# Optimization experiments

Hardware: AMD Instinct MI355X
Metric: run time of the kernel (lower is better)

Reference implementation:

```python
import jax, jax.numpy as jnp
import numpy as np

TEMP = 0.01  # temperature_att_sc


def grid_sample_bilinear(img, grid):
    """torch.nn.functional.grid_sample, mode='bilinear', padding_mode='zeros',
    align_corners=False. img: (B,C,H,W); grid: (B,Hg,Wg,2) with (x,y) coords."""
    B, C, H, W = img.shape
    gx, gy = grid[..., 0], grid[..., 1]            # (B,Hg,Wg)
    ix = ((gx + 1.0) * W - 1.0) * 0.5              # unnormalize (align_corners=False)
    iy = ((gy + 1.0) * H - 1.0) * 0.5
    ix0 = jnp.floor(ix); iy0 = jnp.floor(iy)
    ix1 = ix0 + 1.0;     iy1 = iy0 + 1.0
    wx1 = ix - ix0; wx0 = 1.0 - wx1
    wy1 = iy - iy0; wy0 = 1.0 - wy1
    flat = img.reshape(B, C, H * W)
    Hg, Wg = gx.shape[1], gx.shape[2]

    def gather(iy_, ix_):
        valid = (ix_ >= 0) & (ix_ <= W - 1) & (iy_ >= 0) & (iy_ <= H - 1)
        ixc = jnp.clip(ix_, 0, W - 1).astype(jnp.int32)
        iyc = jnp.clip(iy_, 0, H - 1).astype(jnp.int32)
        idx = (iyc * W + ixc).reshape(B, 1, Hg * Wg)
        vals = jnp.take_along_axis(flat, jnp.broadcast_to(idx, (B, C, Hg * Wg)), axis=2)
        vals = vals.reshape(B, C, Hg, Wg)
        return vals * valid[:, None, :, :].astype(img.dtype)

    out = (gather(iy0, ix0) * (wy0 * wx0)[:, None]
         + gather(iy0, ix1) * (wy0 * wx1)[:, None]
         + gather(iy1, ix0) * (wy1 * wx0)[:, None]
         + gather(iy1, ix1) * (wy1 * wx1)[:, None])
    return out


def setup_inputs() -> dict:
    key = jax.random.key(0)
    ks = jax.random.split(key, 16)
    B, S, D = 256, 197, 768
    H60 = 60
    std = 0.02
    inp = {
        "x": jax.random.normal(ks[0], (B, S, D), dtype=jnp.float32),
        "mask": jnp.zeros((B, S), dtype=jnp.float32),
        "Wq": jax.random.normal(ks[1], (D, D), dtype=jnp.float32) * std,
        "bq": jnp.zeros((D,), dtype=jnp.float32),
        "Wk": jax.random.normal(ks[2], (D, D), dtype=jnp.float32) * std,
        "bk": jnp.zeros((D,), dtype=jnp.float32),
        "Wv": jax.random.normal(ks[3], (D, D), dtype=jnp.float32) * std,
        "bv": jnp.zeros((D,), dtype=jnp.float32),
        "W1": jax.random.normal(ks[4], (H60, 2 * D), dtype=jnp.float32) * std,
        "b1": jnp.zeros((H60,), dtype=jnp.float32),
        "W2": jax.random.normal(ks[5], (H60, H60), dtype=jnp.float32) * std,
        "b2": jnp.zeros((H60,), dtype=jnp.float32),
        "W3": jax.random.normal(ks[6], (2, H60), dtype=jnp.float32) * std,
        "b3": jnp.zeros((2,), dtype=jnp.float32),
    }
    return inp


def reference(x, mask, Wq, bq, Wk, bk, Wv, bv, W1, b1, W2, b2, W3, b3):
    B, S, D = x.shape
    G = int(np.sqrt(S))  # grid_dim; S = G*G + 1 (class token)
    q = jnp.einsum('bsd,ed->bse', x, Wq) + bq
    k = jnp.einsum('bsd,ed->bse', x, Wk) + bk
    v = jnp.einsum('bsd,ed->bse', x, Wv) + bv
    k_nc = k[:, 1:, :]          # (B, G*G, D)
    v_nc = v[:, 1:, :]
    q_nc = q[:, 1:, :]
    k_img = jnp.transpose(k_nc, (0, 2, 1)).reshape(B, D, G, G)
    v_img = jnp.transpose(v_nc, (0, 2, 1)).reshape(B, D, G, G)
    # key_net_2D MLP -> per-patch sampling offsets in [0,1]
    h = jnp.concatenate((q_nc, k_nc), axis=2)       # (B, G*G, 2D)
    h = jax.nn.relu(jnp.einsum('bse,fe->bsf', h, W1) + b1)
    h = jax.nn.relu(jnp.einsum('bse,fe->bsf', h, W2) + b2)
    sample = jax.nn.sigmoid(jnp.einsum('bse,fe->bsf', h, W3) + b3)  # (B, G*G, 2)
    sample_x = sample[:, :, 0:1]
    sample_y = sample[:, :, 1:2]
    grid = jnp.concatenate((sample_x, sample_y), axis=1).reshape(B, G, G, 2)
    sk = grid_sample_bilinear(k_img, grid)          # (B, D, G, G)
    sv = grid_sample_bilinear(v_img, grid)
    sk = jnp.transpose(sk.reshape(B, D, G * G), (0, 2, 1))  # (B, G*G, D)
    sv = jnp.transpose(sv.reshape(B, D, G * G), (0, 2, 1))
    cls = jnp.ones((B, 1, D), dtype=x.dtype)
    sk = jnp.concatenate((cls, sk), axis=1)         # (B, S, D)
    sv = jnp.concatenate((cls, sv), axis=1)
    scores = jnp.sum(sk * q, axis=-1)               # (B, S)
    attention = jax.nn.sigmoid(TEMP * scores)[:, :, None] * sv
    return attention
```

## Files before the change

kernel.cpp:

```cpp
#include <hip/hip_runtime.h>
#include <hip/hip_bf16.h>
#include <stdint.h>

#define TEMP 0.01f

typedef __attribute__((ext_vector_type(8))) short short8;
typedef __attribute__((ext_vector_type(4))) float f32x4;
typedef __attribute__((ext_vector_type(2))) float f32x2;

__device__ __forceinline__ ushort f2bf(float f) {
  union { float f; uint32_t u; } c; c.f = f;
  uint32_t u = c.u;
  uint32_t r = (u + 0x7FFFu + ((u >> 16) & 1u)) >> 16;
  return (ushort)r;
}
__device__ __forceinline__ float bf2f(ushort h) {
  union { uint32_t u; float f; } c; c.u = ((uint32_t)h) << 16;
  return c.f;
}

__device__ __forceinline__ void async16(void* lds, const void* g) {
  __builtin_amdgcn_global_load_lds(
      (const __attribute__((address_space(1))) uint32_t*)g,
      (__attribute__((address_space(3))) uint32_t*)lds,
      16, 0, 0);
}

__global__ __launch_bounds__(256) void convert_all(
    const float* __restrict__ X, ushort* __restrict__ Xb,
    const float* __restrict__ Wq, const float* __restrict__ Wk, const float* __restrict__ Wv,
    const float* __restrict__ bq, const float* __restrict__ bk, const float* __restrict__ bv,
    const float* __restrict__ W1, const float* __restrict__ b1,
    ushort* __restrict__ wqkv, ushort* __restrict__ w1p,
    float* __restrict__ biasq, float* __restrict__ b1p) {
  int idx = blockIdx.x * 256 + threadIdx.x;
  int stride = gridDim.x * 256;
  for (int i = idx; i < 9682944; i += stride) {
    float4 f = ((const float4*)X)[i];
    ushort4 u;
    u.x = f2bf(f.x); u.y = f2bf(f.y); u.z = f2bf(f.z); u.w = f2bf(f.w);
    ((ushort4*)Xb)[i] = u;
  }
  for (int i = idx; i < 2304 * 768; i += stride) {
    int row = i / 768;
    float v = (row < 768) ? Wq[i] : (row < 1536) ? Wk[i - 768 * 768] : Wv[i - 1536 * 768];
    wqkv[i] = f2bf(v);
  }
  for (int i = idx; i < 64 * 1536; i += stride) {
    int row = i / 1536;
    w1p[i] = f2bf(row < 60 ? W1[i] : 0.f);
  }
  for (int i = idx; i < 2304; i += stride)
    biasq[i] = (i < 768) ? bq[i] : (i < 1536) ? bk[i - 768] : bv[i - 1536];
  for (int i = idx; i < 64; i += stride)
    b1p[i] = (i < 60) ? b1[i] : 0.f;
}

#define STAGE(LDSBASE, SRC, OFF)                                          \
  async16(smem + (LDSBASE) + ldsW, (SRC) + (OFF));                        \
  async16(smem + (LDSBASE) + 8192 + ldsW, (SRC) + 64 * 1536 + (OFF))

#define RDA4(BASE, F0)                                                                   \
  _Pragma("unroll") for (int f = 0; f < 4; ++f) {                                        \
    a[f][0] = *(const short8*)(smem + (BASE) + aRow + ((F0) + f) * 2048 + c0);           \
    a[f][1] = *(const short8*)(smem + (BASE) + aRow + ((F0) + f) * 2048 + c1);           \
  }
#define RDB2(BASE, G0)                                                                   \
  _Pragma("unroll") for (int g = 0; g < 2; ++g) {                                        \
    b[(G0) + g][0] = *(const short8*)(smem + (BASE) + bRow + ((G0) + g) * 2048 + c0);    \
    b[(G0) + g][1] = *(const short8*)(smem + (BASE) + bRow + ((G0) + g) * 2048 + c1);    \
  }
#define MF16(F0, G0)                                                                     \
  _Pragma("unroll") for (int f = 0; f < 4; ++f)                                          \
  _Pragma("unroll") for (int g = 0; g < 2; ++g) {                                        \
    acc[(F0) + f][(G0) + g] = __builtin_amdgcn_mfma_f32_16x16x32_bf16(                   \
        a[f][0], b[(G0) + g][0], acc[(F0) + f][(G0) + g], 0, 0, 0);                      \
    acc[(F0) + f][(G0) + g] = __builtin_amdgcn_mfma_f32_16x16x32_bf16(                   \
        a[f][1], b[(G0) + g][1], acc[(F0) + f][(G0) + g], 0, 0, 0);                      \
  }
#define PH_OPEN                                          \
  __builtin_amdgcn_s_barrier();                          \
  asm volatile("s_waitcnt lgkmcnt(0)" ::: "memory");     \
  __builtin_amdgcn_s_setprio(1);
#define PH_CLOSE                                         \
  __builtin_amdgcn_s_setprio(0);                         \
  __builtin_amdgcn_s_barrier();

__global__ __launch_bounds__(512, 1) void gemm_qkv(const ushort* __restrict__ Xb,
                                                   const ushort* __restrict__ Wb,
                                                   const float* __restrict__ bias,
                                                   ushort* __restrict__ QKV) {
  __shared__ char smem[131072];
  const int tid = threadIdx.x;
  const int lane = tid & 63;
  const int wv = tid >> 6;
  const int wr = wv >> 2;
  const int wc = wv & 3;
  const int lmod = lane & 15, ldiv = lane >> 4;

  int orig = blockIdx.x;
  int xcd = orig & 7, bidx = orig >> 3;
  int nw = (xcd < 5 ? xcd * 222 : 1110 + (xcd - 5) * 221) + bidx;
  const int m0 = (nw / 9) * 256;
  const int n0 = (nw % 9) * 256;

  const int srow = tid >> 3;
  const int scol = (((tid & 7) ^ (srow & 7)) << 4);
  const char* aS = (const char*)Xb + (size_t)(m0 + srow) * 1536 + scol;
  const char* bS = (const char*)Wb + (size_t)(n0 + srow) * 1536 + scol;
  const int ldsW = wv << 10;

  const int aRow = (wr * 128 + lmod) * 128;
  const int bRow = (wc * 64 + lmod) * 128;
  const int c0 = (ldiv * 16) ^ ((lmod & 7) << 4);
  const int c1 = (64 + ldiv * 16) ^ ((lmod & 7) << 4);

  const int AE = 0, AO = 32768, BE = 65536, BO = 98304;

  f32x4 acc[8][4] = {};

  STAGE(AE, aS, 0);
  STAGE(AE + 16384, aS + 128 * 1536, 0);
  STAGE(BE, bS, 0);
  STAGE(BE + 16384, bS + 128 * 1536, 0);
  STAGE(AO, aS, 128);
  asm volatile("s_waitcnt vmcnt(2)" ::: "memory");
  __builtin_amdgcn_s_barrier();

  for (int i = 0; i < 6; ++i) {
    const int kb1 = i * 256 + 128;
    const int kb2 = i * 256 + 256;
    const int kb3 = i * 256 + 384;
    const bool more = (i < 5);

    short8 a[4][2], b[4][2];
    RDA4(AE, 0); RDB2(BE, 0);
    STAGE(AO + 16384, aS + 128 * 1536, kb1);
    PH_OPEN; MF16(0, 0); PH_CLOSE;
    RDB2(BE, 2);
    STAGE(BO, bS, kb1);
    PH_OPEN; MF16(0, 2); PH_CLOSE;
    RDA4(AE, 4);
    STAGE(BO + 16384, bS + 128 * 1536, kb1);
    PH_OPEN; MF16(4, 0); PH_CLOSE;
    if (more) { STAGE(AE, aS, kb2); }
    PH_OPEN; MF16(4, 2);
    __builtin_amdgcn_s_setprio(0);
    if (more) { asm volatile("s_waitcnt vmcnt(2)" ::: "memory"); }
    else      { asm volatile("s_waitcnt vmcnt(0)" ::: "memory"); }
    __builtin_amdgcn_s_barrier();
    RDA4(AO, 0); RDB2(BO, 0);
    if (more) { STAGE(AE + 16384, aS + 128 * 1536, kb2); }
    PH_OPEN; MF16(0, 0); PH_CLOSE;
    RDB2(BO, 2);
    if (more) { STAGE(BE, bS, kb2); }
    PH_OPEN; MF16(0, 2); PH_CLOSE;
    RDA4(AO, 4);
    if (more) { STAGE(BE + 16384, bS + 128 * 1536, kb2); }
    PH_OPEN; MF16(4, 0); PH_CLOSE;
    if (more) { STAGE(AO, aS, kb3); }
    PH_OPEN; MF16(4, 2);
    __builtin_amdgcn_s_setprio(0);
    if (more) { asm volatile("s_waitcnt vmcnt(2)" ::: "memory"); }
    __builtin_amdgcn_s_barrier();
  }

#pragma unroll
  for (int f = 0; f < 8; ++f) {
    int row = m0 + wr * 128 + f * 16 + ldiv * 4;
#pragma unroll
    for (int g = 0; g < 4; ++g) {
      int col = n0 + wc * 64 + g * 16 + lmod;
      float bs = bias[col];
#pragma unroll
      for (int rr = 0; rr < 4; ++rr)
        QKV[(size_t)(row + rr) * 2304 + col] = f2bf(acc[f][g][rr] + bs);
    }
  }
}

__global__ __launch_bounds__(256) void gemm_mlp(const ushort* __restrict__ QKV,
                                                const ushort* __restrict__ W1p,
                                                const float* __restrict__ b1p,
                                                const float* __restrict__ W2,
                                                const float* __restrict__ b2,
                                                const float* __restrict__ W3,
                                                const float* __restrict__ b3,
                                                float* __restrict__ SAMPLE) {
  __shared__ char smem[32032];
  float* sW2 = (float*)(smem + 16896);
  float* sW3 = (float*)(smem + 31296);
  float* sb2 = (float*)(smem + 31776);
  float* sb3 = (float*)(smem + 32016);
  const int tid = threadIdx.x;
  const int lane = tid & 63;
  const int wv = tid >> 6;
  const int p0 = blockIdx.x * 128;
  const int lmod = lane & 15, ldiv = lane >> 4;

  for (int i = tid; i < 3600; i += 256) sW2[i] = W2[i];
  for (int i = tid; i < 120; i += 256) sW3[i] = W3[i];
  if (tid < 60) sb2[tid] = b2[tid];
  if (tid < 2) sb3[tid] = b3[tid];

  f32x4 acc[2][4] = {};
  const ushort* As = (const ushort*)smem;
  const ushort* Bs = (const ushort*)(smem + 8192);

  const int r = tid >> 2, cb = (tid & 3) * 16;
  int p_a = p0 + r;
  int p_b = p0 + 64 + r;
  int grow_a = (p_a / 196) * 197 + 1 + (p_a % 196);
  int grow_b = (p_b / 196) * 197 + 1 + (p_b % 196);
  const char* gA0 = (const char*)QKV + (size_t)grow_a * 4608 + cb;
  const char* gA1 = (const char*)QKV + (size_t)grow_b * 4608 + cb;
  const char* gB = (const char*)W1p + (size_t)r * 3072 + cb;

  for (int k0 = 0; k0 < 1536; k0 += 32) {
    int kb = k0 * 2;
    async16(smem + wv * 1024,        gA0 + kb);
    async16(smem + 4096 + wv * 1024, gA1 + kb);
    async16(smem + 8192 + wv * 1024, gB + kb);
    __syncthreads();

    short8 a[2], b[4];
    a[0] = *(const short8*)(As + (wv * 32 + lmod) * 32 + ldiv * 8);
    a[1] = *(const short8*)(As + (wv * 32 + 16 + lmod) * 32 + ldiv * 8);
#pragma unroll
    for (int j = 0; j < 4; ++j)
      b[j] = *(const short8*)(Bs + (j * 16 + lmod) * 32 + ldiv * 8);
#pragma unroll
    for (int i = 0; i < 2; ++i)
#pragma unroll
      for (int j = 0; j < 4; ++j)
        acc[i][j] = __builtin_amdgcn_mfma_f32_16x16x32_bf16(a[i], b[j], acc[i][j], 0, 0, 0);
    __syncthreads();
  }

  ushort* Hs = (ushort*)smem;
#pragma unroll
  for (int i = 0; i < 2; ++i) {
    int lrow = wv * 32 + i * 16 + ldiv * 4;
#pragma unroll
    for (int j = 0; j < 4; ++j) {
      int col = j * 16 + lmod;
      float bs = b1p[col];
#pragma unroll
      for (int rr = 0; rr < 4; ++rr) {
        float v = fmaxf(acc[i][j][rr] + bs, 0.f);
        Hs[(lrow + rr) * 66 + col] = f2bf(v);
      }
    }
  }
  __syncthreads();

  const int plocal = tid >> 1;
  const int half = tid & 1;
  const uint32_t* hrow = (const uint32_t*)(Hs + plocal * 66);
  float h[60];
#pragma unroll
  for (int i = 0; i < 30; ++i) {
    uint32_t u = hrow[i];
    h[2 * i] = bf2f((ushort)(u & 0xffffu));
    h[2 * i + 1] = bf2f((ushort)(u >> 16));
  }
  float s0 = 0.f, s1 = 0.f;
  const int obase = half * 30;
  for (int oo = 0; oo < 30; ++oo) {
    int o = obase + oo;
    float a = sb2[o];
    const float4* wrow = (const float4*)(sW2 + o * 60);
#pragma unroll
    for (int k = 0; k < 15; ++k) {
      float4 w4 = wrow[k];
      a += h[4 * k] * w4.x + h[4 * k + 1] * w4.y + h[4 * k + 2] * w4.z + h[4 * k + 3] * w4.w;
    }
    a = fmaxf(a, 0.f);
    s0 += a * sW3[o];
    s1 += a * sW3[60 + o];
  }
  s0 += __shfl_xor(s0, 1, 64);
  s1 += __shfl_xor(s1, 1, 64);
  if (half == 0) {
    int p = p0 + plocal;
    SAMPLE[2 * p]     = 1.f / (1.f + __expf(-(s0 + sb3[0])));
    SAMPLE[2 * p + 1] = 1.f / (1.f + __expf(-(s1 + sb3[1])));
  }
}

__global__ __launch_bounds__(256) void sample_attn(const ushort* __restrict__ QKV,
                                                   const float* __restrict__ SAMPLE,
                                                   float* __restrict__ OUT) {
  int tid = threadIdx.x, lane = tid & 63, wv = tid >> 6;
  int orig = blockIdx.x;
  int nw = (orig & 7) * 1576 + (orig >> 3);
  int pos = nw * 4 + wv;
  int b = pos / 197, s = pos % 197;

  const uint32_t* qrow = (const uint32_t*)(QKV + (size_t)pos * 2304);
  float qv[12];
#pragma unroll
  for (int j = 0; j < 6; ++j) {
    uint32_t u = qrow[lane + j * 64];
    qv[2 * j] = bf2f((ushort)(u & 0xffffu));
    qv[2 * j + 1] = bf2f((ushort)(u >> 16));
  }

  float sk[12], sv[12];
#pragma unroll
  for (int j = 0; j < 12; ++j) { sk[j] = 0.f; sv[j] = 0.f; }

  if (s == 0) {
#pragma unroll
    for (int j = 0; j < 12; ++j) { sk[j] = 1.f; sv[j] = 1.f; }
  } else {
    int g = s - 1;
    int t0 = 2 * g, t1 = 2 * g + 1;
    const float* smp = SAMPLE + (size_t)b * 392;
    float gx = (t0 < 196) ? smp[2 * t0] : smp[2 * (t0 - 196) + 1];
    float gy = (t1 < 196) ? smp[2 * t1] : smp[2 * (t1 - 196) + 1];
    float ix = ((gx + 1.f) * 14.f - 1.f) * 0.5f;
    float iy = ((gy + 1.f) * 14.f - 1.f) * 0.5f;
    float fx0 = floorf(ix), fy0 = floorf(iy);
    float wx1 = ix - fx0, wx0 = 1.f - wx1;
    float wy1 = iy - fy0, wy0 = 1.f - wy1;
    int x0 = (int)fx0, x1 = x0 + 1, y0 = (int)fy0, y1 = y0 + 1;
    float w[4] = {wy0 * wx0, wy0 * wx1, wy1 * wx0, wy1 * wx1};
    int xs[4] = {x0, x1, x0, x1};
    int ys[4] = {y0, y0, y1, y1};
#pragma unroll
    for (int c = 0; c < 4; ++c) {
      bool valid = (xs[c] >= 0) && (xs[c] <= 13) && (ys[c] >= 0) && (ys[c] <= 13);
      float wc = valid ? w[c] : 0.f;
      int xc = min(max(xs[c], 0), 13);
      int yc = min(max(ys[c], 0), 13);
      const uint32_t* krow =
          (const uint32_t*)(QKV + ((size_t)(b * 197 + 1 + yc * 14 + xc) * 2304 + 768));
      const uint32_t* vrow = krow + 384;
#pragma unroll
      for (int j = 0; j < 6; ++j) {
        uint32_t ku = krow[lane + j * 64];
        uint32_t vu = vrow[lane + j * 64];
        sk[2 * j]     += wc * bf2f((ushort)(ku & 0xffffu));
        sk[2 * j + 1] += wc * bf2f((ushort)(ku >> 16));
        sv[2 * j]     += wc * bf2f((ushort)(vu & 0xffffu));
        sv[2 * j + 1] += wc * bf2f((ushort)(vu >> 16));
      }
    }
  }

  float part = 0.f;
#pragma unroll
  for (int j = 0; j < 12; ++j) part += sk[j] * qv[j];
#pragma unroll
  for (int m = 1; m < 64; m <<= 1) part += __shfl_xor(part, m, 64);
  float sig = 1.f / (1.f + __expf(-TEMP * part));

  float* orow = OUT + (size_t)pos * 768;
#pragma unroll
  for (int j = 0; j < 6; ++j) {
    f32x2 o;
    o.x = sig * sv[2 * j];
    o.y = sig * sv[2 * j + 1];
    __builtin_nontemporal_store(o, (f32x2*)(orow + 2 * lane + 128 * j));
  }
}

extern "C" void kernel_launch(void* const* d_in, const int* in_sizes, int n_in,
                              void* d_out, int out_size, void* d_ws, size_t ws_size,
                              hipStream_t stream) {
  const float* x  = (const float*)d_in[0];
  const float* Wq = (const float*)d_in[2];
  const float* bq = (const float*)d_in[3];
  const float* Wk = (const float*)d_in[4];
  const float* bk = (const float*)d_in[5];
  const float* Wv = (const float*)d_in[6];
  const float* bv = (const float*)d_in[7];
  const float* W1 = (const float*)d_in[8];
  const float* b1 = (const float*)d_in[9];
  const float* W2 = (const float*)d_in[10];
  const float* b2 = (const float*)d_in[11];
  const float* W3 = (const float*)d_in[12];
  const float* b3 = (const float*)d_in[13];
  float* out = (float*)d_out;

  char* ws = (char*)d_ws;
  ushort* x_bf = (ushort*)ws;   ws += 77463552;
  ushort* qkv = (ushort*)ws;    ws += 232390656;
  ushort* wqkv = (ushort*)ws;   ws += 3538944;
  ushort* w1p = (ushort*)ws;    ws += 196608;
  float* biasq = (float*)ws;    ws += 9216;
  float* b1p = (float*)ws;      ws += 256;
  float* sample = (float*)ws;   ws += 401408;

  convert_all<<<2048, 256, 0, stream>>>(x, x_bf, Wq, Wk, Wv, bq, bk, bv, W1, b1,
                                        wqkv, w1p, biasq, b1p);
  gemm_qkv<<<1773, 512, 0, stream>>>(x_bf, wqkv, biasq, qkv);
  gemm_mlp<<<392, 256, 0, stream>>>(qkv, w1p, b1p, W2, b2, W3, b3, sample);
  sample_attn<<<12608, 256, 0, stream>>>(qkv, sample, out);
}
```

Baseline: 345.3 us.

## Make QKV GEMM persistent with cross-tile prefetch of next tile's first K block

The QKV GEMM now launches 256 blocks, one per CU, instead of one block per output tile. Each block loops over tiles strided by 256 and keeps the same XCD-aware tile mapping. During the last K iteration of a tile it issues the global-to-LDS loads for the next tile's first K slices, so the pipeline prologue is hidden between tiles. This removes the per-block launch and pipeline ramp-up cost, but the bias-add and store epilogue is still not overlapped and the loop control adds some complexity.

```diff
diff --git a/kernel.cpp b/kernel.cpp
--- a/kernel.cpp
+++ b/kernel.cpp
@@ -86,6 +86,13 @@
   __builtin_amdgcn_s_setprio(0);                         \
   __builtin_amdgcn_s_barrier();
 
+__device__ __forceinline__ void tilecoord(int orig, int& m0, int& n0) {
+  int xcd = orig & 7, idx = orig >> 3;
+  int nw = (xcd < 5 ? xcd * 222 : 1110 + (xcd - 5) * 221) + idx;
+  m0 = (nw / 9) * 256;
+  n0 = (nw % 9) * 256;
+}
+
 __global__ __launch_bounds__(512, 1) void gemm_qkv(const ushort* __restrict__ Xb,
                                                    const ushort* __restrict__ Wb,
                                                    const float* __restrict__ bias,
@@ -97,17 +104,11 @@
   const int wr = wv >> 2;
   const int wc = wv & 3;
   const int lmod = lane & 15, ldiv = lane >> 4;
-
-  int orig = blockIdx.x;
-  int xcd = orig & 7, bidx = orig >> 3;
-  int nw = (xcd < 5 ? xcd * 222 : 1110 + (xcd - 5) * 221) + bidx;
-  const int m0 = (nw / 9) * 256;
-  const int n0 = (nw % 9) * 256;
+  const int bid = blockIdx.x;
+  const int ntiles = (1772 - bid) / 256 + 1;
 
   const int srow = tid >> 3;
   const int scol = (((tid & 7) ^ (srow & 7)) << 4);
-  const char* aS = (const char*)Xb + (size_t)(m0 + srow) * 1536 + scol;
-  const char* bS = (const char*)Wb + (size_t)(n0 + srow) * 1536 + scol;
   const int ldsW = wv << 10;
 
   const int aRow = (wr * 128 + lmod) * 128;
@@ -116,6 +117,11 @@
   const int c1 = (64 + ldiv * 16) ^ ((lmod & 7) << 4);
 
   const int AE = 0, AO = 32768, BE = 65536, BO = 98304;
+
+  int m0, n0;
+  tilecoord(bid, m0, n0);
+  const char* aS = (const char*)Xb + (size_t)(m0 + srow) * 1536 + scol;
+  const char* bS = (const char*)Wb + (size_t)(n0 + srow) * 1536 + scol;
 
   f32x4 acc[8][4] = {};
 
@@ -127,55 +133,76 @@
   asm volatile("s_waitcnt vmcnt(2)" ::: "memory");
   __builtin_amdgcn_s_barrier();
 
-  for (int i = 0; i < 6; ++i) {
-    const int kb1 = i * 256 + 128;
-    const int kb2 = i * 256 + 256;
-    const int kb3 = i * 256 + 384;
-    const bool more = (i < 5);
-
-    short8 a[4][2], b[4][2];
-    RDA4(AE, 0); RDB2(BE, 0);
-    STAGE(AO + 16384, aS + 128 * 1536, kb1);
-    PH_OPEN; MF16(0, 0); PH_CLOSE;
-    RDB2(BE, 2);
-    STAGE(BO, bS, kb1);
-    PH_OPEN; MF16(0, 2); PH_CLOSE;
-    RDA4(AE, 4);
-    STAGE(BO + 16384, bS + 128 * 1536, kb1);
-    PH_OPEN; MF16(4, 0); PH_CLOSE;
-    if (more) { STAGE(AE, aS, kb2); }
-    PH_OPEN; MF16(4, 2);
-    __builtin_amdgcn_s_setprio(0);
-    if (more) { asm volatile("s_waitcnt vmcnt(2)" ::: "memory"); }
-    else      { asm volatile("s_waitcnt vmcnt(0)" ::: "memory"); }
-    __builtin_amdgcn_s_barrier();
-    RDA4(AO, 0); RDB2(BO, 0);
-    if (more) { STAGE(AE + 16384, aS + 128 * 1536, kb2); }
-    PH_OPEN; MF16(0, 0); PH_CLOSE;
-    RDB2(BO, 2);
-    if (more) { STAGE(BE, bS, kb2); }
-    PH_OPEN; MF16(0, 2); PH_CLOSE;
-    RDA4(AO, 4);
-    if (more) { STAGE(BE + 16384, bS + 128 * 1536, kb2); }
-    PH_OPEN; MF16(4, 0); PH_CLOSE;
-    if (more) { STAGE(AO, aS, kb3); }
-    PH_OPEN; MF16(4, 2);
-    __builtin_amdgcn_s_setprio(0);
-    if (more) { asm volatile("s_waitcnt vmcnt(2)" ::: "memory"); }
-    __builtin_amdgcn_s_barrier();
-  }
-
-#pragma unroll
-  for (int f = 0; f < 8; ++f) {
-    int row = m0 + wr * 128 + f * 16 + ldiv * 4;
-#pragma unroll
-    for (int g = 0; g < 4; ++g) {
-      int col = n0 + wc * 64 + g * 16 + lmod;
-      float bs = bias[col];
-#pragma unroll
-      for (int rr = 0; rr < 4; ++rr)
-        QKV[(size_t)(row + rr) * 2304 + col] = f2bf(acc[f][g][rr] + bs);
-    }
+  for (int t = 0;; ++t) {
+    const bool lastT = (t == ntiles - 1);
+    int m0n = 0, n0n = 0;
+    const char* aS2 = aS;
+    const char* bS2 = bS;
+    if (!lastT) {
+      tilecoord(bid + 256 * (t + 1), m0n, n0n);
+      aS2 = (const char*)Xb + (size_t)(m0n + srow) * 1536 + scol;
+      bS2 = (const char*)Wb + (size_t)(n0n + srow) * 1536 + scol;
+    }
+
+    for (int i = 0; i < 6; ++i) {
+      const int kb1 = i * 256 + 128;
+      const bool ib = (i == 5);
+      const bool stg = !(ib && lastT);
+      const char* pA = ib ? aS2 : aS;
+      const char* pB = ib ? bS2 : bS;
+      const int kA = ib ? 0 : i * 256 + 256;
+
+      short8 a[4][2], b[4][2];
+      RDA4(AE, 0); RDB2(BE, 0);
+      STAGE(AO + 16384, aS + 128 * 1536, kb1);
+      PH_OPEN; MF16(0, 0); PH_CLOSE;
+      RDB2(BE, 2);
+      STAGE(BO, bS, kb1);
+      PH_OPEN; MF16(0, 2); PH_CLOSE;
+      RDA4(AE, 4);
+      STAGE(BO + 16384, bS + 128 * 1536, kb1);
+      PH_OPEN; MF16(4, 0); PH_CLOSE;
+      if (stg) { STAGE(AE, pA, kA); }
+      PH_OPEN; MF16(4, 2);
+      __builtin_amdgcn_s_setprio(0);
+      if (stg) { asm volatile("s_waitcnt vmcnt(2)" ::: "memory"); }
+      else     { asm volatile("s_waitcnt vmcnt(0)" ::: "memory"); }
+      __builtin_amdgcn_s_barrier();
+      RDA4(AO, 0); RDB2(BO, 0);
+      if (stg) { STAGE(AE + 16384, pA + 128 * 1536, kA); }
+      PH_OPEN; MF16(0, 0); PH_CLOSE;
+      RDB2(BO, 2);
+      if (stg) { STAGE(BE, pB, kA); }
+      PH_OPEN; MF16(0, 2); PH_CLOSE;
+      RDA4(AO, 4);
+      if (stg) { STAGE(BE + 16384, pB + 128 * 1536, kA); }
+      PH_OPEN; MF16(4, 0); PH_CLOSE;
+      if (stg) { STAGE(AO, pA, kA + 128); }
+      PH_OPEN; MF16(4, 2);
+      __builtin_amdgcn_s_setprio(0);
+      if (stg) { asm volatile("s_waitcnt vmcnt(2)" ::: "memory"); }
+      __builtin_amdgcn_s_barrier();
+    }
+
+#pragma unroll
+    for (int f = 0; f < 8; ++f) {
+      int row = m0 + wr * 128 + f * 16 + ldiv * 4;
+#pragma unroll
+      for (int g = 0; g < 4; ++g) {
+        int col = n0 + wc * 64 + g * 16 + lmod;
+        float bs = bias[col];
+#pragma unroll
+        for (int rr = 0; rr < 4; ++rr)
+          QKV[(size_t)(row + rr) * 2304 + col] = f2bf(acc[f][g][rr] + bs);
+      }
+    }
+    if (lastT) break;
+#pragma unroll
+    for (int f = 0; f < 8; ++f)
+#pragma unroll
+      for (int g = 0; g < 4; ++g)
+        acc[f][g] = f32x4{0.f, 0.f, 0.f, 0.f};
+    m0 = m0n; n0 = n0n; aS = aS2; bS = bS2;
   }
 }
 
@@ -395,7 +422,7 @@
 
   convert_all<<<2048, 256, 0, stream>>>(x, x_bf, Wq, Wk, Wv, bq, bk, bv, W1, b1,
                                         wqkv, w1p, biasq, b1p);
-  gemm_qkv<<<1773, 512, 0, stream>>>(x_bf, wqkv, biasq, qkv);
+  gemm_qkv<<<256, 512, 0, stream>>>(x_bf, wqkv, biasq, qkv);
   gemm_mlp<<<392, 256, 0, stream>>>(qkv, w1p, b1p, W2, b2, W3, b3, sample);
   sample_attn<<<12608, 256, 0, stream>>>(qkv, sample, out);
 }
```

New measurement: 337.7 us. 2.2% less time.
